# Kernel tuning notes

Measured on AMD Instinct MI355X. Metric: run time of the kernel, lower is better.

The kernel has to match this reference:

```python
import jax, jax.numpy as jnp
import numpy as np

B, T, D = 8, 1024, 16
QUANTILE = 0.5
EPS_T = 1e-6


def setup_inputs() -> dict:
    key = jax.random.key(0)
    k1, k2 = jax.random.split(key)
    z = jax.random.normal(k1, (B, T, D), dtype=jnp.float32)
    variances = jax.random.uniform(k2, (B, T, D), dtype=jnp.float32)
    length_scales = jnp.ones((D,), dtype=jnp.float32)  # nn.Parameter init
    sigmas = jnp.ones((D,), dtype=jnp.float32)         # nn.Parameter init
    return {"z": z, "variances": variances,
            "length_scales": length_scales, "sigmas": sigmas}


def reference(z, variances, length_scales, sigmas):
    b, t, d = z.shape
    dt = z.dtype
    N = b * t
    zf = z.reshape(N, d)          # [N, D] flattened per-dim samples
    vf = variances.reshape(N, d)  # [N, D]

    # quantile-threshold mask per latent dim (linear-interp quantile, as torch)
    thr = jnp.quantile(vf, QUANTILE, axis=0)          # [D]
    m = (vf <= thr).astype(dt)                        # [N, D] 0/1 mask

    # time index for every flattened point: arange(T) tiled over batch
    tt = jnp.tile(jnp.arange(t, dtype=dt), b)         # [N]
    # pairwise weight W_ij = 1 / (|t_i - t_j| + eps); shared across dims
    W = 1.0 / (jnp.abs(tt[:, None] - tt[None, :]) + EPS_T)  # [N, N]

    # masked pairwise mean of (z_i - z_j)^2 * W_ij, algebraically:
    #   sum_ij m_i m_j (z_i - z_j)^2 W_ij = 2 (u^T W m - v^T W v)
    # with u = m*z^2, v = m*z (diagonal contributes 0 since m^2 = m).
    V = m * zf                                        # [N, D]
    U = V * zf                                        # [N, D]
    WM = W @ jnp.concatenate([m, V], axis=1)          # [N, 2D] single GEMM
    Wm, WV = WM[:, :d], WM[:, d:]
    S = 2.0 * (jnp.sum(U * Wm, axis=0) - jnp.sum(V * WV, axis=0))  # [D]

    n = jnp.sum(m, axis=0)                            # [D] selected counts
    mean_ratio = S / (n * n)                          # mean over N_sel^2 pairs
    ls_est = jax.lax.stop_gradient(jnp.sqrt(mean_ratio))  # .detach() in torch

    # (unbiased variance estimate; only used for 'cauchy' kernel, kept for parity)
    mu = jnp.sum(V, axis=0) / n
    var_est = jax.lax.stop_gradient(
        jnp.sum(m * (zf - mu[None, :]) ** 2, axis=0) / (n - 1.0))

    enough = n >= 2.0
    length_scale = jnp.where(enough, ls_est, jnp.exp(length_scales))  # [D]
    _sigma = jnp.where(enough, var_est, jnp.exp(sigmas))  # unused for rbf

    # rbf kernel per dim: exp(-(ti - tj)^2 / ls^2), [D, T, T]
    ts = jnp.arange(t, dtype=dt)
    dist2 = (ts[None, :] - ts[:, None]) ** 2          # [T, T]
    K = jnp.exp(-dist2[None, :, :] / (length_scale[:, None, None] ** 2))
    # repeat over batch -> [B, D, T, T] (covariance of the MVN prior; loc is 0)
    return jnp.broadcast_to(K[None], (b, d, t, t))
```

## Files before the change

kernel.cpp:

```cpp
#include <hip/hip_runtime.h>

typedef float vfloat4 __attribute__((ext_vector_type(4)));

#define TT 1024
#define BB 8
#define DD 16
#define NN 8192

__global__ __launch_bounds__(1024) void median_k(const float* __restrict__ v,
                                                 float* __restrict__ thr) {
    __shared__ float s[NN];
    const int d = blockIdx.x;
    for (int i = threadIdx.x; i < NN; i += 1024) s[i] = v[i * DD + d];
    __syncthreads();
    for (int k = 2; k <= NN; k <<= 1) {
        for (int j = k >> 1; j > 0; j >>= 1) {
            for (int i = threadIdx.x; i < NN; i += 1024) {
                int l = i ^ j;
                if (l > i) {
                    float a = s[i], b = s[l];
                    bool up = ((i & k) == 0);
                    if ((a > b) == up) { s[i] = b; s[l] = a; }
                }
            }
            __syncthreads();
        }
    }
    if (threadIdx.x == 0) thr[d] = 0.5f * (s[NN / 2 - 1] + s[NN / 2]);
}

__global__ __launch_bounds__(256) void colsum_k(const float* __restrict__ z,
                                                const float* __restrict__ v,
                                                const float* __restrict__ thr,
                                                float* __restrict__ ms,
                                                float* __restrict__ vs,
                                                float* __restrict__ us) {
    const int g = blockIdx.x * 256 + threadIdx.x;
    const int d = g & (DD - 1);
    const float t = thr[d];
    float sm = 0.f, sv = 0.f, su = 0.f;
#pragma unroll
    for (int b = 0; b < BB; ++b) {
        float vv = v[b * (TT * DD) + g];
        float zz = z[b * (TT * DD) + g];
        if (vv <= t) { sm += 1.f; sv += zz; su += zz * zz; }
    }
    ms[g] = sm; vs[g] = sv; us[g] = su;
}

__global__ __launch_bounds__(1024) void scale_k(const float* __restrict__ ms,
                                                const float* __restrict__ vs,
                                                const float* __restrict__ us,
                                                const float* __restrict__ lsin,
                                                float* __restrict__ inv_out) {
    __shared__ float sm[TT], sv[TT], wt[TT], red[1024];
    const int d = blockIdx.x;
    const int p = threadIdx.x;
    sm[p] = ms[p * DD + d];
    sv[p] = vs[p * DD + d];
    wt[p] = 1.0f / ((float)p + 1e-6f);
    const float a = us[p * DD + d];
    __syncthreads();
    const float c = sv[p];
    float acc = 0.f;
#pragma unroll 4
    for (int q = 0; q < TT; ++q) {
        int ad = p - q; ad = ad < 0 ? -ad : ad;
        acc += wt[ad] * (a * sm[q] - c * sv[q]);
    }
    red[p] = acc;
    __syncthreads();
    for (int off = 512; off > 0; off >>= 1) {
        if (p < off) red[p] += red[p + off];
        __syncthreads();
    }
    const float S2 = 2.0f * red[0];
    __syncthreads();
    red[p] = sm[p];
    __syncthreads();
    for (int off = 512; off > 0; off >>= 1) {
        if (p < off) red[p] += red[p + off];
        __syncthreads();
    }
    if (p == 0) {
        const float n = red[0];
        float ls;
        if (n >= 2.0f) ls = sqrtf(S2 / (n * n));
        else           ls = expf(lsin[d]);
        inv_out[d] = 1.0f / (ls * ls);
    }
}

__global__ __launch_bounds__(256) void write_k(const float* __restrict__ inv_ls2,
                                               float* __restrict__ out) {
    const int bid = blockIdx.x;
    const int d = bid >> 10;
    const int i = bid & (TT - 1);
    const float inv = inv_ls2[d];
    const int j0 = threadIdx.x * 4;
    vfloat4 val;
#pragma unroll
    for (int jj = 0; jj < 4; ++jj) {
        const int diff = (j0 + jj) - i;
        const float f = (float)(diff * diff);
        val[jj] = __expf(-f * inv);
    }
    const size_t base = ((size_t)d << 20) | ((size_t)i << 10) | (size_t)j0;
#pragma unroll
    for (int b = 0; b < BB; ++b) {
        vfloat4* p = (vfloat4*)(out + ((size_t)b << 24) + base);
        __builtin_nontemporal_store(val, p);
    }
}

extern "C" void kernel_launch(void* const* d_in, const int* in_sizes, int n_in,
                              void* d_out, int out_size, void* d_ws, size_t ws_size,
                              hipStream_t stream) {
    const float* z    = (const float*)d_in[0];
    const float* v    = (const float*)d_in[1];
    const float* lsin = (const float*)d_in[2];
    float* out = (float*)d_out;

    float* ws  = (float*)d_ws;
    float* thr = ws;
    float* inv = ws + 16;
    float* ms  = ws + 32;
    float* vs  = ms + TT * DD;
    float* us  = vs + TT * DD;

    median_k<<<DD, 1024, 0, stream>>>(v, thr);
    colsum_k<<<(TT * DD) / 256, 256, 0, stream>>>(z, v, thr, ms, vs, us);
    scale_k<<<DD, 1024, 0, stream>>>(ms, vs, us, lsin, inv);
    write_k<<<DD * TT, 256, 0, stream>>>(inv, out);
}
```

Before: 686.4 us.

## Replace bitonic-sort median with radix select and split scale reduction across blocks

The median kernel no longer runs a full bitonic sort of 8192 values in shared memory. It now finds the 4096th element with three histogram radix-select passes over order-preserving integer keys, plus a final pass that locates the next key up. The scale kernel is split into 256 blocks of 64 threads that each reduce with wave shuffles and combine through global float atomics, and a tiny extra kernel computes the inverse length scale. This cuts median cost and spreads the pairwise sum over more CUs, at the price of one more launch and an atomic summation order that is not deterministic.

```diff
diff --git a/kernel.cpp b/kernel.cpp
--- a/kernel.cpp
+++ b/kernel.cpp
@@ -7,26 +7,93 @@
 #define DD 16
 #define NN 8192
 
+__device__ inline float untr(unsigned u) {
+    unsigned b = (u & 0x80000000u) ? (u & 0x7fffffffu) : ~u;
+    return __uint_as_float(b);
+}
+
 __global__ __launch_bounds__(1024) void median_k(const float* __restrict__ v,
                                                  float* __restrict__ thr) {
-    __shared__ float s[NN];
+    __shared__ unsigned key[NN];
+    __shared__ unsigned hist[2048];
+    __shared__ unsigned wsum[16];
+    __shared__ unsigned found_bin, found_cum;
+    __shared__ unsigned s_cle, s_min;
     const int d = blockIdx.x;
-    for (int i = threadIdx.x; i < NN; i += 1024) s[i] = v[i * DD + d];
+    const int tid = threadIdx.x;
+    const int wid = tid >> 6, lane = tid & 63;
+
+    for (int i = tid; i < NN; i += 1024) {
+        unsigned b = __float_as_uint(v[i * DD + d]);
+        key[i] = (b & 0x80000000u) ? ~b : (b | 0x80000000u);
+    }
+    if (tid == 0) { s_cle = 0; s_min = 0xFFFFFFFFu; }
     __syncthreads();
-    for (int k = 2; k <= NN; k <<= 1) {
-        for (int j = k >> 1; j > 0; j >>= 1) {
-            for (int i = threadIdx.x; i < NN; i += 1024) {
-                int l = i ^ j;
-                if (l > i) {
-                    float a = s[i], b = s[l];
-                    bool up = ((i & k) == 0);
-                    if ((a > b) == up) { s[i] = b; s[l] = a; }
-                }
+
+    unsigned prefix = 0;
+    unsigned r = 4095;
+    int matched_bits = 0;
+    int shift = 32;
+    const int chunk_bits[3] = {11, 11, 10};
+#pragma unroll
+    for (int pass = 0; pass < 3; ++pass) {
+        const int bits = chunk_bits[pass];
+        shift -= bits;
+        const int nb = 1 << bits;
+        hist[tid] = 0; hist[tid + 1024] = 0;
+        __syncthreads();
+        for (int i = tid; i < NN; i += 1024) {
+            unsigned k = key[i];
+            if (matched_bits == 0 || (k >> (shift + bits)) == prefix)
+                atomicAdd(&hist[(k >> shift) & (unsigned)(nb - 1)], 1u);
+        }
+        __syncthreads();
+        unsigned h0 = 0, h1 = 0, s2 = 0;
+        if (tid < nb / 2) { h0 = hist[2 * tid]; h1 = hist[2 * tid + 1]; s2 = h0 + h1; }
+        unsigned inc = s2;
+        for (int o = 1; o < 64; o <<= 1) {
+            unsigned t = __shfl_up(inc, o);
+            if (lane >= o) inc += t;
+        }
+        if (lane == 63) wsum[wid] = inc;
+        __syncthreads();
+        if (tid < 16) {
+            unsigned x = wsum[tid], ix = x;
+            for (int o = 1; o < 16; o <<= 1) {
+                unsigned t = __shfl_up(ix, o);
+                if (lane >= o) ix += t;
             }
-            __syncthreads();
-        }
-    }
-    if (threadIdx.x == 0) thr[d] = 0.5f * (s[NN / 2 - 1] + s[NN / 2]);
+            wsum[tid] = ix - x;
+        }
+        __syncthreads();
+        if (tid < nb / 2) {
+            unsigned cum = wsum[wid] + (inc - s2);
+            if (r >= cum && r < cum + h0)            { found_bin = 2u * tid;     found_cum = cum; }
+            else if (r >= cum + h0 && r < cum + s2)  { found_bin = 2u * tid + 1; found_cum = cum + h0; }
+        }
+        __syncthreads();
+        prefix = (prefix << bits) | found_bin;
+        r -= found_cum;
+        matched_bits += bits;
+    }
+    const unsigned A = prefix;
+
+    unsigned cle = 0, mg = 0xFFFFFFFFu;
+    for (int i = tid; i < NN; i += 1024) {
+        unsigned k = key[i];
+        if (k <= A) cle++;
+        else mg = min(mg, k);
+    }
+    for (int o = 32; o; o >>= 1) {
+        cle += __shfl_xor(cle, o);
+        mg = min(mg, (unsigned)__shfl_xor(mg, o));
+    }
+    if (lane == 0) { atomicAdd(&s_cle, cle); atomicMin(&s_min, mg); }
+    __syncthreads();
+    if (tid == 0) {
+        unsigned Bk = (s_cle >= 4097u) ? A : s_min;
+        thr[d] = 0.5f * (untr(A) + untr(Bk));
+    }
 }
 
 __global__ __launch_bounds__(256) void colsum_k(const float* __restrict__ z,
@@ -34,8 +101,14 @@
                                                 const float* __restrict__ thr,
                                                 float* __restrict__ ms,
                                                 float* __restrict__ vs,
-                                                float* __restrict__ us) {
+                                                float* __restrict__ us,
+                                                float* __restrict__ Sacc,
+                                                float* __restrict__ nacc) {
     const int g = blockIdx.x * 256 + threadIdx.x;
+    if (blockIdx.x == 0) {
+        if (threadIdx.x < DD)            Sacc[threadIdx.x] = 0.f;
+        else if (threadIdx.x < 2 * DD)   nacc[threadIdx.x - DD] = 0.f;
+    }
     const int d = g & (DD - 1);
     const float t = thr[d];
     float sm = 0.f, sv = 0.f, su = 0.f;
@@ -48,46 +121,52 @@
     ms[g] = sm; vs[g] = sv; us[g] = su;
 }
 
-__global__ __launch_bounds__(1024) void scale_k(const float* __restrict__ ms,
-                                                const float* __restrict__ vs,
-                                                const float* __restrict__ us,
-                                                const float* __restrict__ lsin,
-                                                float* __restrict__ inv_out) {
-    __shared__ float sm[TT], sv[TT], wt[TT], red[1024];
-    const int d = blockIdx.x;
-    const int p = threadIdx.x;
-    sm[p] = ms[p * DD + d];
-    sv[p] = vs[p * DD + d];
-    wt[p] = 1.0f / ((float)p + 1e-6f);
+__global__ __launch_bounds__(64) void scale_k(const float* __restrict__ ms,
+                                              const float* __restrict__ vs,
+                                              const float* __restrict__ us,
+                                              float* __restrict__ Sacc,
+                                              float* __restrict__ nacc) {
+    __shared__ float sm[TT], sv[TT], wt[TT];
+    const int d = blockIdx.x >> 4;
+    const int chunk = blockIdx.x & 15;
+    const int tid = threadIdx.x;
+    for (int q = tid; q < TT; q += 64) {
+        sm[q] = ms[q * DD + d];
+        sv[q] = vs[q * DD + d];
+        wt[q] = 1.0f / ((float)q + 1e-6f);
+    }
+    __syncthreads();
+    const int p = chunk * 64 + tid;
     const float a = us[p * DD + d];
-    __syncthreads();
     const float c = sv[p];
     float acc = 0.f;
 #pragma unroll 4
     for (int q = 0; q < TT; ++q) {
         int ad = p - q; ad = ad < 0 ? -ad : ad;
-        acc += wt[ad] * (a * sm[q] - c * sv[q]);
-    }
-    red[p] = acc;
-    __syncthreads();
-    for (int off = 512; off > 0; off >>= 1) {
-        if (p < off) red[p] += red[p + off];
-        __syncthreads();
-    }
-    const float S2 = 2.0f * red[0];
-    __syncthreads();
-    red[p] = sm[p];
-    __syncthreads();
-    for (int off = 512; off > 0; off >>= 1) {
-        if (p < off) red[p] += red[p + off];
-        __syncthreads();
-    }
-    if (p == 0) {
-        const float n = red[0];
-        float ls;
-        if (n >= 2.0f) ls = sqrtf(S2 / (n * n));
-        else           ls = expf(lsin[d]);
-        inv_out[d] = 1.0f / (ls * ls);
+        acc = fmaf(wt[ad], fmaf(a, sm[q], -(c * sv[q])), acc);
+    }
+    float npart = sm[p];
+    for (int o = 32; o; o >>= 1) {
+        acc += __shfl_xor(acc, o);
+        npart += __shfl_xor(npart, o);
+    }
+    if (tid == 0) {
+        atomicAdd(&Sacc[d], 2.0f * acc);
+        atomicAdd(&nacc[d], npart);
+    }
+}
+
+__global__ __launch_bounds__(64) void ls_k(const float* __restrict__ Sacc,
+                                           const float* __restrict__ nacc,
+                                           const float* __restrict__ lsin,
+                                           float* __restrict__ inv_out) {
+    const int d = threadIdx.x;
+    if (d < DD) {
+        const float n = nacc[d], S = Sacc[d];
+        float invv;
+        if (n >= 2.0f) invv = (n * n) / S;
+        else { const float e = expf(lsin[d]); invv = 1.0f / (e * e); }
+        inv_out[d] = invv;
     }
 }
 
@@ -121,15 +200,18 @@
     const float* lsin = (const float*)d_in[2];
     float* out = (float*)d_out;
 
-    float* ws  = (float*)d_ws;
-    float* thr = ws;
-    float* inv = ws + 16;
-    float* ms  = ws + 32;
-    float* vs  = ms + TT * DD;
-    float* us  = vs + TT * DD;
+    float* ws   = (float*)d_ws;
+    float* thr  = ws;
+    float* inv  = ws + 16;
+    float* Sacc = ws + 32;
+    float* nacc = ws + 48;
+    float* ms   = ws + 64;
+    float* vs   = ms + TT * DD;
+    float* us   = vs + TT * DD;
 
     median_k<<<DD, 1024, 0, stream>>>(v, thr);
-    colsum_k<<<(TT * DD) / 256, 256, 0, stream>>>(z, v, thr, ms, vs, us);
-    scale_k<<<DD, 1024, 0, stream>>>(ms, vs, us, lsin, inv);
+    colsum_k<<<(TT * DD) / 256, 256, 0, stream>>>(z, v, thr, ms, vs, us, Sacc, nacc);
+    scale_k<<<DD * 16, 64, 0, stream>>>(ms, vs, us, Sacc, nacc);
+    ls_k<<<1, 64, 0, stream>>>(Sacc, nacc, lsin, inv);
     write_k<<<DD * TT, 256, 0, stream>>>(inv, out);
 }
```

Measured after the change: 574.5 us. 16.3% less time.
